# Kernel optimization log

Measured on AMD Instinct MI355X. Metric: run time of the kernel, lower is better.

The kernel has to match this reference:

```python
import jax, jax.numpy as jnp
import numpy as np

B, S, DM, H, DK, R, THETA = 8, 2048, 512, 8, 64, 128, 10000.0
BLK = R          # key/query block size; window radius == block size
NB = S // BLK    # number of blocks
NEG = -1e30      # additive mask for invalid positions (fp32-safe)


def setup_inputs() -> dict:
    key = jax.random.key(0)
    ks = jax.random.split(key, 5)
    scale = 0.02
    hidden_states = jax.random.normal(ks[0], (B, S, DM), jnp.float32)
    Wq = jax.random.normal(ks[1], (DM, H * DK), jnp.float32) * scale
    Wk = jax.random.normal(ks[2], (DM, H * DK), jnp.float32) * scale
    Wv = jax.random.normal(ks[3], (DM, H * DK), jnp.float32) * scale
    Wo = jax.random.normal(ks[4], (H * DK, DM), jnp.float32) * scale
    position_ids = jnp.tile(jnp.arange(S, dtype=jnp.int64)[None, :], (B, 1))
    return {"hidden_states": hidden_states, "Wq": Wq, "Wk": Wk, "Wv": Wv,
            "Wo": Wo, "position_ids": position_ids}


def _apply_rope(q, k, position_ids):
    # q,k: [B,H,S,DK]; position_ids: [B,S]
    half = DK // 2
    inv_freq = 1.0 / (THETA ** (jnp.arange(0, DK, 2, dtype=jnp.float32) / DK))  # [half]
    freqs = position_ids.astype(jnp.float32)[:, :, None] * inv_freq[None, None, :]  # [B,S,half]
    emb = jnp.concatenate([freqs, freqs], axis=-1)        # [B,S,DK]
    cos = jnp.cos(emb)[:, None, :, :]                     # [B,1,S,DK]
    sin = jnp.sin(emb)[:, None, :, :]

    def rotate_half(x):
        return jnp.concatenate([-x[..., half:], x[..., :half]], axis=-1)

    return q * cos + rotate_half(q) * sin, k * cos + rotate_half(k) * sin


def _band_mask():
    # valid[nb, BLK, 3*BLK]: key within [0,S) and |j - i| <= R
    b = jnp.arange(NB)[:, None, None]
    qi = jnp.arange(BLK)[None, :, None]
    kj = jnp.arange(3 * BLK)[None, None, :]
    kglob = (b - 1) * BLK + kj                 # global key index
    qglob = b * BLK + qi                        # global query index
    return (jnp.abs(kglob - qglob) <= R) & (kglob >= 0) & (kglob < S)


def reference(hidden_states, Wq, Wk, Wv, Wo, position_ids):
    # projections: [B,S,DM] -> [B,H,S,DK]
    def shape(x):
        return x.reshape(B, S, H, DK).transpose(0, 2, 1, 3)

    q = shape(hidden_states @ Wq)
    k = shape(hidden_states @ Wk)
    v = shape(hidden_states @ Wv)
    q, k = _apply_rope(q, k, position_ids)

    # block-banded sliding-window attention, softmax_scale = 1.0 (no scaling)
    pad = ((0, 0), (0, 0), (BLK, BLK), (0, 0))
    kb = jnp.pad(k, pad).reshape(B, H, NB + 2, BLK, DK)
    vb = jnp.pad(v, pad).reshape(B, H, NB + 2, BLK, DK)
    # neighbor window: blocks [b-1, b, b+1] -> [B,H,NB,3*BLK,DK]
    kwin = jnp.concatenate([kb[:, :, i:i + NB] for i in range(3)], axis=3)
    vwin = jnp.concatenate([vb[:, :, i:i + NB] for i in range(3)], axis=3)
    qb = q.reshape(B, H, NB, BLK, DK)

    scores = jnp.einsum('bhnqd,bhnkd->bhnqk', qb, kwin)   # unscaled
    valid = _band_mask()                                  # [NB,BLK,3*BLK]
    scores = jnp.where(valid[None, None], scores, NEG)
    attn = jax.nn.softmax(scores.astype(jnp.float32), axis=-1).astype(scores.dtype)
    outb = jnp.einsum('bhnqk,bhnkd->bhnqd', attn, vwin)   # [B,H,NB,BLK,DK]

    out = outb.reshape(B, H, S, DK).transpose(0, 2, 1, 3).reshape(B, S, H * DK)
    return out @ Wo
```

## Files before the change

kernel.cpp:

```cpp
#include <hip/hip_runtime.h>

using bf16 = __bf16;
typedef __bf16 bf16x8 __attribute__((ext_vector_type(8)));
typedef __bf16 bf16x4 __attribute__((ext_vector_type(4)));
typedef float f32x4 __attribute__((ext_vector_type(4)));
typedef float f32x16 __attribute__((ext_vector_type(16)));

#define MFMA16(a, b, c) __builtin_amdgcn_mfma_f32_16x16x32_bf16((a), (b), (c), 0, 0, 0)
#define MFMA32(a, b, c) __builtin_amdgcn_mfma_f32_32x32x16_bf16((a), (b), (c), 0, 0, 0)

constexpr int S = 2048, DM = 512, H = 8, DK = 64, HD = 512;
constexpr int NBLK = 16, BLK = 128;
constexpr int Mrows = 8 * S;
constexpr float LOG2E = 1.44269504088896340736f;

__device__ __forceinline__ void gll16(const void* g, void* l) {
  __builtin_amdgcn_global_load_lds((const __attribute__((address_space(1))) unsigned int*)g,
                                   (__attribute__((address_space(3))) unsigned int*)l, 16, 0, 0);
}

__global__ void k_conv(const float* __restrict__ x, bf16* __restrict__ y) {
  size_t i = ((size_t)blockIdx.x * 256 + threadIdx.x) * 8;
  float4 a = *(const float4*)(x + i);
  float4 b = *(const float4*)(x + i + 4);
  bf16x8 o;
  o[0] = (bf16)a.x; o[1] = (bf16)a.y; o[2] = (bf16)a.z; o[3] = (bf16)a.w;
  o[4] = (bf16)b.x; o[5] = (bf16)b.y; o[6] = (bf16)b.z; o[7] = (bf16)b.w;
  *(bf16x8*)(y + i) = o;
}

__global__ void k_transw4(const float* __restrict__ W0, const float* __restrict__ W1,
                          const float* __restrict__ W2, const float* __restrict__ W3,
                          bf16* __restrict__ D0, bf16* __restrict__ D1,
                          bf16* __restrict__ D2, bf16* __restrict__ D3) {
  const int z = blockIdx.z;
  const float* W = (z == 0) ? W0 : (z == 1) ? W1 : (z == 2) ? W2 : W3;
  bf16* Wt = (z == 0) ? D0 : (z == 1) ? D1 : (z == 2) ? D2 : D3;
  __shared__ float tile[32][33];
  int k0 = blockIdx.x * 32, n0 = blockIdx.y * 32;
  int tx = threadIdx.x, ty = threadIdx.y;
#pragma unroll
  for (int i = 0; i < 4; i++)
    tile[ty * 4 + i][tx] = W[(size_t)(k0 + ty * 4 + i) * 512 + n0 + tx];
  __syncthreads();
#pragma unroll
  for (int i = 0; i < 4; i++)
    Wt[(size_t)(n0 + ty * 4 + i) * 512 + k0 + tx] = (bf16)tile[tx][ty * 4 + i];
}

__global__ void k_ctab(float2* __restrict__ ctab) {
  int idx = blockIdx.x * 256 + threadIdx.x;
  int s = idx >> 5, i = idx & 31;
  float invf = exp2f(-(float)i * (13.287712379549449f / 32.0f));
  float ang = (float)s * invf;
  ctab[idx] = make_float2(cosf(ang), sinf(ang));
}

__global__ __launch_bounds__(256) void k_gemm_qkv(
    const bf16* __restrict__ Xb,
    const bf16* __restrict__ Wtq, const bf16* __restrict__ Wtk, const bf16* __restrict__ Wtv,
    bf16* __restrict__ Qo, bf16* __restrict__ Ko, bf16* __restrict__ Vt,
    const float2* __restrict__ ctab) {
  const int z = blockIdx.z;
  const bf16* Wt = (z == 0) ? Wtq : ((z == 1) ? Wtk : Wtv);
  bf16* dst = (z == 0) ? Qo : Ko;
  const float qscale = (z == 0) ? LOG2E : 1.0f;

  __shared__ __align__(16) char Asm[128 * 64];
  __shared__ __align__(16) char Bsm[128 * 64];

  const int t = threadIdx.x, l = t & 63, wid = t >> 6;
  const int l15 = l & 15, l4 = l >> 4;
  const int wm = wid >> 1, wn = wid & 1;
  const size_t arow0 = (size_t)blockIdx.x * 128;
  const size_t brow0 = (size_t)blockIdx.y * 128;

  f32x4 acc[4][4] = {};
  const int rs = wid * 16 + (l >> 2);
  const int cs = (l & 3) ^ ((l >> 2) & 3);

  for (int kt = 0; kt < 16; ++kt) {
    const int k0 = kt * 32;
    __syncthreads();
    gll16(Xb + (arow0 + rs) * 512 + k0 + cs * 8,      Asm + wid * 1024);
    gll16(Xb + (arow0 + 64 + rs) * 512 + k0 + cs * 8, Asm + 4096 + wid * 1024);
    gll16(Wt + (brow0 + rs) * 512 + k0 + cs * 8,      Bsm + wid * 1024);
    gll16(Wt + (brow0 + 64 + rs) * 512 + k0 + cs * 8, Bsm + 4096 + wid * 1024);
    __syncthreads();
    bf16x8 af[4], bfr[4];
#pragma unroll
    for (int mi = 0; mi < 4; mi++) {
      int row = wm * 64 + mi * 16 + l15;
      af[mi] = *(const bf16x8*)(Asm + row * 64 + ((l4 ^ (row & 3)) * 16));
    }
#pragma unroll
    for (int ni = 0; ni < 4; ni++) {
      int row = wn * 64 + ni * 16 + l15;
      bfr[ni] = *(const bf16x8*)(Bsm + row * 64 + ((l4 ^ (row & 3)) * 16));
    }
#pragma unroll
    for (int mi = 0; mi < 4; mi++)
#pragma unroll
      for (int ni = 0; ni < 4; ni++)
        acc[mi][ni] = MFMA16(af[mi], bfr[ni], acc[mi][ni]);
  }

  if (z == 2) {
    const int b = (int)(arow0 >> 11);
#pragma unroll
    for (int mi = 0; mi < 4; mi++) {
      int scol = (int)(arow0 & 2047) + wm * 64 + mi * 16 + l4 * 4;
#pragma unroll
      for (int ni = 0; ni < 4; ni++) {
        int col = (int)brow0 + wn * 64 + ni * 16 + l15;
        int hh = col >> 6, dd = col & 63;
        bf16x4 pk = {(bf16)acc[mi][ni][0], (bf16)acc[mi][ni][1],
                     (bf16)acc[mi][ni][2], (bf16)acc[mi][ni][3]};
        *(bf16x4*)(Vt + ((size_t)((b * H + hh) * 64 + dd)) * 2048 + scol) = pk;
      }
    }
    return;
  }

#pragma unroll
  for (int mi = 0; mi < 4; mi++) {
#pragma unroll
    for (int r = 0; r < 4; r++) {
      int grow = (int)arow0 + wm * 64 + mi * 16 + l4 * 4 + r;
      size_t rowoff = (size_t)grow * 512 + brow0 + wn * 64;
      int s = grow & (S - 1);
      float2 cs0 = ctab[s * 32 + l15];
      float2 cs1 = ctab[s * 32 + 16 + l15];
#pragma unroll
      for (int ni = 0; ni < 4; ni++) {
        float a = acc[mi][ni][r];
        float b = acc[mi][ni ^ 2][r];
        float2 cc = (ni & 1) ? cs1 : cs0;
        float val = (ni < 2) ? (a * cc.x - b * cc.y) : (a * cc.x + b * cc.y);
        dst[rowoff + ni * 16 + l15] = (bf16)(val * qscale);
      }
    }
  }
}

__global__ __launch_bounds__(256) void k_gemm_out(
    const bf16* __restrict__ A, const bf16* __restrict__ Wt, float* __restrict__ out) {
  __shared__ __align__(16) char Asm[128 * 64];
  __shared__ __align__(16) char Bsm[128 * 64];

  const int t = threadIdx.x, l = t & 63, wid = t >> 6;
  const int l15 = l & 15, l4 = l >> 4;
  const int wm = wid >> 1, wn = wid & 1;
  const size_t arow0 = (size_t)blockIdx.x * 128;
  const size_t brow0 = (size_t)blockIdx.y * 128;

  f32x4 acc[4][4] = {};
  const int rs = wid * 16 + (l >> 2);
  const int cs = (l & 3) ^ ((l >> 2) & 3);

  for (int kt = 0; kt < 16; ++kt) {
    const int k0 = kt * 32;
    __syncthreads();
    gll16(A + (arow0 + rs) * 512 + k0 + cs * 8,       Asm + wid * 1024);
    gll16(A + (arow0 + 64 + rs) * 512 + k0 + cs * 8,  Asm + 4096 + wid * 1024);
    gll16(Wt + (brow0 + rs) * 512 + k0 + cs * 8,      Bsm + wid * 1024);
    gll16(Wt + (brow0 + 64 + rs) * 512 + k0 + cs * 8, Bsm + 4096 + wid * 1024);
    __syncthreads();
    bf16x8 af[4], bfr[4];
#pragma unroll
    for (int mi = 0; mi < 4; mi++) {
      int row = wm * 64 + mi * 16 + l15;
      af[mi] = *(const bf16x8*)(Asm + row * 64 + ((l4 ^ (row & 3)) * 16));
    }
#pragma unroll
    for (int ni = 0; ni < 4; ni++) {
      int row = wn * 64 + ni * 16 + l15;
      bfr[ni] = *(const bf16x8*)(Bsm + row * 64 + ((l4 ^ (row & 3)) * 16));
    }
#pragma unroll
    for (int mi = 0; mi < 4; mi++)
#pragma unroll
      for (int ni = 0; ni < 4; ni++)
        acc[mi][ni] = MFMA16(af[mi], bfr[ni], acc[mi][ni]);
  }

#pragma unroll
  for (int mi = 0; mi < 4; mi++)
#pragma unroll
    for (int r = 0; r < 4; r++) {
      int grow = (int)arow0 + wm * 64 + mi * 16 + l4 * 4 + r;
      size_t rowoff = (size_t)grow * 512 + brow0 + wn * 64;
#pragma unroll
      for (int ni = 0; ni < 4; ni++)
        out[rowoff + ni * 16 + l15] = acc[mi][ni][r];
    }
}

__global__ __launch_bounds__(256, 4) void k_attn(
    const bf16* __restrict__ Q, const bf16* __restrict__ K, const bf16* __restrict__ Vt,
    bf16* __restrict__ O) {
  const int bid = blockIdx.x;
  const int swz = (bid & 7) * 128 + (bid >> 3);
  const int nb = swz & 15, h = (swz >> 4) & 7, bb = swz >> 7;
  const int t = threadIdx.x, l = t & 63, w = t >> 6;
  const int q31 = l & 31, hi = l >> 5;

  const int bh = bb * H + h;
  const size_t qrow = (size_t)bb * S + nb * BLK + w * 32 + q31;

  const bf16* Qp = Q + qrow * HD + h * DK + hi * 8;
  bf16x8 qb[4];
#pragma unroll
  for (int ks = 0; ks < 4; ks++) qb[ks] = *(const bf16x8*)(Qp + ks * 16);

  f32x16 o0 = {}, o1 = {};
  float mrun = -3e38f, lrun = 0.f;

  const bf16* Kbase = K + (size_t)bb * S * HD + h * DK + hi * 8;
  const bf16* Vbase = Vt + ((size_t)bh * 64 + q31) * 2048 + hi * 8;
  const int s0 = nb * BLK + w * 32 - 128;

  auto pv = [&](const f32x16& p, int kgc) {
    unsigned int Wd[4][2];
#pragma unroll
    for (int a = 0; a < 4; a++)
#pragma unroll
      for (int b2 = 0; b2 < 2; b2++) {
        unsigned int wd;
        asm("v_cvt_pk_bf16_f32 %0, %1, %2" : "=v"(wd) : "v"(p[4 * a + 2 * b2]), "v"(p[4 * a + 2 * b2 + 1]));
        Wd[a][b2] = wd;
      }
    bf16x8 pf[2];
#pragma unroll
    for (int ks = 0; ks < 2; ks++) {
      union { unsigned int u[4]; bf16x8 v; } cvt;
#pragma unroll
      for (int b2 = 0; b2 < 2; b2++) {
        unsigned int low_w = Wd[2 * ks][b2];
        unsigned int hi_w  = Wd[2 * ks + 1][b2];
        unsigned int msg = hi ? low_w : hi_w;
        unsigned int rec = __shfl_xor(msg, 32);
        cvt.u[b2]     = hi ? rec : low_w;
        cvt.u[2 + b2] = hi ? hi_w : rec;
      }
      pf[ks] = cvt.v;
    }
    const bf16* Vp = Vbase + kgc;
    o0 = MFMA32(*(const bf16x8*)(Vp), pf[0], o0);
    o0 = MFMA32(*(const bf16x8*)(Vp + 16), pf[1], o0);
    o1 = MFMA32(*(const bf16x8*)(Vp + 32 * 2048), pf[0], o1);
    o1 = MFMA32(*(const bf16x8*)(Vp + 32 * 2048 + 16), pf[1], o1);
  };

#pragma unroll
  for (int st = 0; st < 5; ++st) {
    const bool has2 = (st < 4);
    const int c0 = st * 2, c1 = c0 + 1;
    const int kg0 = s0 + c0 * 32, kg1 = s0 + c1 * 32;
    const int kc0 = kg0 < 0 ? 0 : (kg0 > S - 32 ? S - 32 : kg0);
    const int kc1 = kg1 < 0 ? 0 : (kg1 > S - 32 ? S - 32 : kg1);

    f32x16 a0 = {}, a1 = {};
    {
      const bf16* Kp = Kbase + (size_t)(kc0 + q31) * HD;
      a0 = MFMA32(*(const bf16x8*)(Kp),      qb[0], a0);
      a0 = MFMA32(*(const bf16x8*)(Kp + 16), qb[1], a0);
      a0 = MFMA32(*(const bf16x8*)(Kp + 32), qb[2], a0);
      a0 = MFMA32(*(const bf16x8*)(Kp + 48), qb[3], a0);
    }
    if (has2) {
      const bf16* Kp = Kbase + (size_t)(kc1 + q31) * HD;
      a1 = MFMA32(*(const bf16x8*)(Kp),      qb[0], a1);
      a1 = MFMA32(*(const bf16x8*)(Kp + 16), qb[1], a1);
      a1 = MFMA32(*(const bf16x8*)(Kp + 32), qb[2], a1);
      a1 = MFMA32(*(const bf16x8*)(Kp + 48), qb[3], a1);
    }

    if (kg0 != kc0) {
#pragma unroll
      for (int rg = 0; rg < 16; rg++) a0[rg] = -1e30f;
    } else if (c0 == 0) {
#pragma unroll
      for (int rg = 0; rg < 16; rg++) {
        int kk = (rg & 3) + 8 * (rg >> 2) + 4 * hi;
        if (kk < q31) a0[rg] = -1e30f;
      }
    } else if (c0 == 8) {
#pragma unroll
      for (int rg = 0; rg < 16; rg++) {
        int kk = (rg & 3) + 8 * (rg >> 2) + 4 * hi;
        if (kk > q31) a0[rg] = -1e30f;
      }
    }
    if (has2 && kg1 != kc1) {
#pragma unroll
      for (int rg = 0; rg < 16; rg++) a1[rg] = -1e30f;
    }

    f32x16 mx = a0;
    if (has2) {
#pragma unroll
      for (int rg = 0; rg < 16; rg++) mx[rg] = fmaxf(mx[rg], a1[rg]);
    }
#pragma unroll
    for (int sl = 8; sl >= 1; sl >>= 1)
#pragma unroll
      for (int i = 0; i < sl; i++) mx[i] = fmaxf(mx[i], mx[i + sl]);
    const float pm = fmaxf(mx[0], __shfl_xor(mx[0], 32));

    if (!__all(pm - mrun <= 8.0f)) {
      const float mnew = fmaxf(mrun, pm);
      const float alpha = exp2f(mrun - mnew);
      lrun *= alpha;
#pragma unroll
      for (int rg = 0; rg < 16; rg++) { o0[rg] *= alpha; o1[rg] *= alpha; }
      mrun = mnew;
    }

    float rsum = 0.f;
#pragma unroll
    for (int rg = 0; rg < 16; rg++) { a0[rg] = exp2f(a0[rg] - mrun); rsum += a0[rg]; }
    if (has2) {
#pragma unroll
      for (int rg = 0; rg < 16; rg++) { a1[rg] = exp2f(a1[rg] - mrun); rsum += a1[rg]; }
    }
    rsum += __shfl_xor(rsum, 32);
    lrun += rsum;

    pv(a0, kc0);
    if (has2) pv(a1, kc1);
  }

  const float inv = 1.0f / lrun;
  bf16* Op = O + qrow * HD + h * DK + 4 * hi;
#pragma unroll
  for (int dt = 0; dt < 2; dt++) {
    const f32x16 oo = dt ? o1 : o0;
#pragma unroll
    for (int a = 0; a < 4; a++) {
      bf16x4 ob = {(bf16)(oo[4 * a + 0] * inv), (bf16)(oo[4 * a + 1] * inv),
                   (bf16)(oo[4 * a + 2] * inv), (bf16)(oo[4 * a + 3] * inv)};
      *(bf16x4*)(Op + dt * 32 + 8 * a) = ob;
    }
  }
}

extern "C" void kernel_launch(void* const* d_in, const int* in_sizes, int n_in,
                              void* d_out, int out_size, void* d_ws, size_t ws_size,
                              hipStream_t stream) {
  const float* hs = (const float*)d_in[0];
  const float* Wq = (const float*)d_in[1];
  const float* Wk = (const float*)d_in[2];
  const float* Wv = (const float*)d_in[3];
  const float* Wo = (const float*)d_in[4];
  float* out = (float*)d_out;

  char* ws = (char*)d_ws;
  const size_t MB = 1u << 20;
  bf16* Xb = (bf16*)(ws);
  bf16* Qb = (bf16*)(ws + 16 * MB);
  bf16* Kb = (bf16*)(ws + 32 * MB);
  bf16* Vt = (bf16*)(ws + 48 * MB);
  bf16* Wtq = (bf16*)(ws + 64 * MB);
  bf16* Wtk = Wtq + 512 * 512;
  bf16* Wtv = Wtk + 512 * 512;
  bf16* Wto = Wtv + 512 * 512;
  float2* ctab = (float2*)(ws + 64 * MB + 4 * 512 * 512 * sizeof(bf16));
  bf16* AO = Xb;

  k_conv<<<dim3(Mrows * DM / (256 * 8)), dim3(256), 0, stream>>>(hs, Xb);
  k_transw4<<<dim3(16, 16, 4), dim3(32, 8), 0, stream>>>(Wq, Wk, Wv, Wo, Wtq, Wtk, Wtv, Wto);
  k_ctab<<<dim3(S * 32 / 256), dim3(256), 0, stream>>>(ctab);
  k_gemm_qkv<<<dim3(Mrows / 128, 4, 3), dim3(256), 0, stream>>>(Xb, Wtq, Wtk, Wtv, Qb, Kb, Vt, ctab);
  k_attn<<<dim3(NBLK * H * 8), dim3(256), 0, stream>>>(Qb, Kb, Vt, AO);
  k_gemm_out<<<dim3(Mrows / 128, 4), dim3(256), 0, stream>>>(AO, Wto, out);
}
```

Baseline: 117.2 us.

## Double-buffer GEMM LDS tiles and split attention keys across wave pairs

Both projection GEMMs now use double-buffered LDS. The next K-slice is issued through global_load_lds while MFMAs run on the current slice, so one barrier per iteration replaces two. The attention kernel now gives each 32-query group two waves: one handles the first two key chunk pairs and the other handles the rest. The partial softmax states are merged through LDS, which doubles the grid and raises occupancy (launch bounds 6). In exchange it adds LDS traffic and a block-wide sync for the merge, the load is uneven (2 vs 3 steps), and the LDS footprint per block grows.

```diff
diff --git a/kernel.cpp b/kernel.cpp
--- a/kernel.cpp
+++ b/kernel.cpp
@@ -66,8 +66,8 @@
   bf16* dst = (z == 0) ? Qo : Ko;
   const float qscale = (z == 0) ? LOG2E : 1.0f;
 
-  __shared__ __align__(16) char Asm[128 * 64];
-  __shared__ __align__(16) char Bsm[128 * 64];
+  __shared__ __align__(16) char Asm2[2][8192];
+  __shared__ __align__(16) char Bsm2[2][8192];
 
   const int t = threadIdx.x, l = t & 63, wid = t >> 6;
   const int l15 = l & 15, l4 = l >> 4;
@@ -79,30 +79,42 @@
   const int rs = wid * 16 + (l >> 2);
   const int cs = (l & 3) ^ ((l >> 2) & 3);
 
+  auto stage = [&](int kt, int b) {
+    const int k0 = kt * 32;
+    gll16(Xb + (arow0 + rs) * 512 + k0 + cs * 8,      Asm2[b] + wid * 1024);
+    gll16(Xb + (arow0 + 64 + rs) * 512 + k0 + cs * 8, Asm2[b] + 4096 + wid * 1024);
+    gll16(Wt + (brow0 + rs) * 512 + k0 + cs * 8,      Bsm2[b] + wid * 1024);
+    gll16(Wt + (brow0 + 64 + rs) * 512 + k0 + cs * 8, Bsm2[b] + 4096 + wid * 1024);
+  };
+
+  stage(0, 0);
+  asm volatile("s_waitcnt vmcnt(0)" ::: "memory");
+  __builtin_amdgcn_s_barrier();
+
+  int cur = 0;
   for (int kt = 0; kt < 16; ++kt) {
-    const int k0 = kt * 32;
-    __syncthreads();
-    gll16(Xb + (arow0 + rs) * 512 + k0 + cs * 8,      Asm + wid * 1024);
-    gll16(Xb + (arow0 + 64 + rs) * 512 + k0 + cs * 8, Asm + 4096 + wid * 1024);
-    gll16(Wt + (brow0 + rs) * 512 + k0 + cs * 8,      Bsm + wid * 1024);
-    gll16(Wt + (brow0 + 64 + rs) * 512 + k0 + cs * 8, Bsm + 4096 + wid * 1024);
-    __syncthreads();
+    if (kt < 15) stage(kt + 1, cur ^ 1);
     bf16x8 af[4], bfr[4];
 #pragma unroll
     for (int mi = 0; mi < 4; mi++) {
       int row = wm * 64 + mi * 16 + l15;
-      af[mi] = *(const bf16x8*)(Asm + row * 64 + ((l4 ^ (row & 3)) * 16));
+      af[mi] = *(const bf16x8*)(Asm2[cur] + row * 64 + ((l4 ^ (row & 3)) * 16));
     }
 #pragma unroll
     for (int ni = 0; ni < 4; ni++) {
       int row = wn * 64 + ni * 16 + l15;
-      bfr[ni] = *(const bf16x8*)(Bsm + row * 64 + ((l4 ^ (row & 3)) * 16));
+      bfr[ni] = *(const bf16x8*)(Bsm2[cur] + row * 64 + ((l4 ^ (row & 3)) * 16));
     }
 #pragma unroll
     for (int mi = 0; mi < 4; mi++)
 #pragma unroll
       for (int ni = 0; ni < 4; ni++)
         acc[mi][ni] = MFMA16(af[mi], bfr[ni], acc[mi][ni]);
+    if (kt < 15) {
+      asm volatile("s_waitcnt vmcnt(0)" ::: "memory");
+      __builtin_amdgcn_s_barrier();
+    }
+    cur ^= 1;
   }
 
   if (z == 2) {
@@ -145,8 +157,8 @@
 
 __global__ __launch_bounds__(256) void k_gemm_out(
     const bf16* __restrict__ A, const bf16* __restrict__ Wt, float* __restrict__ out) {
-  __shared__ __align__(16) char Asm[128 * 64];
-  __shared__ __align__(16) char Bsm[128 * 64];
+  __shared__ __align__(16) char Asm2[2][8192];
+  __shared__ __align__(16) char Bsm2[2][8192];
 
   const int t = threadIdx.x, l = t & 63, wid = t >> 6;
   const int l15 = l & 15, l4 = l >> 4;
@@ -158,30 +170,42 @@
   const int rs = wid * 16 + (l >> 2);
   const int cs = (l & 3) ^ ((l >> 2) & 3);
 
+  auto stage = [&](int kt, int b) {
+    const int k0 = kt * 32;
+    gll16(A + (arow0 + rs) * 512 + k0 + cs * 8,       Asm2[b] + wid * 1024);
+    gll16(A + (arow0 + 64 + rs) * 512 + k0 + cs * 8,  Asm2[b] + 4096 + wid * 1024);
+    gll16(Wt + (brow0 + rs) * 512 + k0 + cs * 8,      Bsm2[b] + wid * 1024);
+    gll16(Wt + (brow0 + 64 + rs) * 512 + k0 + cs * 8, Bsm2[b] + 4096 + wid * 1024);
+  };
+
+  stage(0, 0);
+  asm volatile("s_waitcnt vmcnt(0)" ::: "memory");
+  __builtin_amdgcn_s_barrier();
+
+  int cur = 0;
   for (int kt = 0; kt < 16; ++kt) {
-    const int k0 = kt * 32;
-    __syncthreads();
-    gll16(A + (arow0 + rs) * 512 + k0 + cs * 8,       Asm + wid * 1024);
-    gll16(A + (arow0 + 64 + rs) * 512 + k0 + cs * 8,  Asm + 4096 + wid * 1024);
-    gll16(Wt + (brow0 + rs) * 512 + k0 + cs * 8,      Bsm + wid * 1024);
-    gll16(Wt + (brow0 + 64 + rs) * 512 + k0 + cs * 8, Bsm + 4096 + wid * 1024);
-    __syncthreads();
+    if (kt < 15) stage(kt + 1, cur ^ 1);
     bf16x8 af[4], bfr[4];
 #pragma unroll
     for (int mi = 0; mi < 4; mi++) {
       int row = wm * 64 + mi * 16 + l15;
-      af[mi] = *(const bf16x8*)(Asm + row * 64 + ((l4 ^ (row & 3)) * 16));
+      af[mi] = *(const bf16x8*)(Asm2[cur] + row * 64 + ((l4 ^ (row & 3)) * 16));
     }
 #pragma unroll
     for (int ni = 0; ni < 4; ni++) {
       int row = wn * 64 + ni * 16 + l15;
-      bfr[ni] = *(const bf16x8*)(Bsm + row * 64 + ((l4 ^ (row & 3)) * 16));
+      bfr[ni] = *(const bf16x8*)(Bsm2[cur] + row * 64 + ((l4 ^ (row & 3)) * 16));
     }
 #pragma unroll
     for (int mi = 0; mi < 4; mi++)
 #pragma unroll
       for (int ni = 0; ni < 4; ni++)
         acc[mi][ni] = MFMA16(af[mi], bfr[ni], acc[mi][ni]);
+    if (kt < 15) {
+      asm volatile("s_waitcnt vmcnt(0)" ::: "memory");
+      __builtin_amdgcn_s_barrier();
+    }
+    cur ^= 1;
   }
 
 #pragma unroll
@@ -196,29 +220,34 @@
     }
 }
 
-__global__ __launch_bounds__(256, 4) void k_attn(
+__global__ __launch_bounds__(256, 6) void k_attn(
     const bf16* __restrict__ Q, const bf16* __restrict__ K, const bf16* __restrict__ Vt,
     bf16* __restrict__ O) {
   const int bid = blockIdx.x;
-  const int swz = (bid & 7) * 128 + (bid >> 3);
-  const int nb = swz & 15, h = (swz >> 4) & 7, bb = swz >> 7;
+  const int swz = (bid & 7) * 256 + (bid >> 3);
+  const int qg = swz & 31, h = (swz >> 5) & 7, bb = swz >> 8;
   const int t = threadIdx.x, l = t & 63, w = t >> 6;
+  const int sub = w & 1, half = w >> 1;
   const int q31 = l & 31, hi = l >> 5;
 
+  __shared__ float Osm[2][64][34];
+  __shared__ float Mlm[2][64][2];
+
   const int bh = bb * H + h;
-  const size_t qrow = (size_t)bb * S + nb * BLK + w * 32 + q31;
+  const int qbase = qg * 64 + sub * 32;
+  const size_t qrow = (size_t)bb * S + qbase + q31;
 
   const bf16* Qp = Q + qrow * HD + h * DK + hi * 8;
-  bf16x8 qb[4];
-#pragma unroll
-  for (int ks = 0; ks < 4; ks++) qb[ks] = *(const bf16x8*)(Qp + ks * 16);
+  bf16x8 qb4[4];
+#pragma unroll
+  for (int ks = 0; ks < 4; ks++) qb4[ks] = *(const bf16x8*)(Qp + ks * 16);
 
   f32x16 o0 = {}, o1 = {};
   float mrun = -3e38f, lrun = 0.f;
 
   const bf16* Kbase = K + (size_t)bb * S * HD + h * DK + hi * 8;
   const bf16* Vbase = Vt + ((size_t)bh * 64 + q31) * 2048 + hi * 8;
-  const int s0 = nb * BLK + w * 32 - 128;
+  const int s0 = qbase - 128;
 
   auto pv = [&](const f32x16& p, int kgc) {
     unsigned int Wd[4][2];
@@ -252,40 +281,38 @@
     o1 = MFMA32(*(const bf16x8*)(Vp + 32 * 2048 + 16), pf[1], o1);
   };
 
-#pragma unroll
-  for (int st = 0; st < 5; ++st) {
-    const bool has2 = (st < 4);
-    const int c0 = st * 2, c1 = c0 + 1;
-    const int kg0 = s0 + c0 * 32, kg1 = s0 + c1 * 32;
+  auto step2 = [&](int c0, bool has2, bool triL, bool triR) {
+    const int kg0 = s0 + c0 * 32, kg1 = kg0 + 32;
+    if ((has2 ? kg1 : kg0) < 0 || kg0 > S - 32) return;
     const int kc0 = kg0 < 0 ? 0 : (kg0 > S - 32 ? S - 32 : kg0);
     const int kc1 = kg1 < 0 ? 0 : (kg1 > S - 32 ? S - 32 : kg1);
 
     f32x16 a0 = {}, a1 = {};
     {
       const bf16* Kp = Kbase + (size_t)(kc0 + q31) * HD;
-      a0 = MFMA32(*(const bf16x8*)(Kp),      qb[0], a0);
-      a0 = MFMA32(*(const bf16x8*)(Kp + 16), qb[1], a0);
-      a0 = MFMA32(*(const bf16x8*)(Kp + 32), qb[2], a0);
-      a0 = MFMA32(*(const bf16x8*)(Kp + 48), qb[3], a0);
+      a0 = MFMA32(*(const bf16x8*)(Kp),      qb4[0], a0);
+      a0 = MFMA32(*(const bf16x8*)(Kp + 16), qb4[1], a0);
+      a0 = MFMA32(*(const bf16x8*)(Kp + 32), qb4[2], a0);
+      a0 = MFMA32(*(const bf16x8*)(Kp + 48), qb4[3], a0);
     }
     if (has2) {
       const bf16* Kp = Kbase + (size_t)(kc1 + q31) * HD;
-      a1 = MFMA32(*(const bf16x8*)(Kp),      qb[0], a1);
-      a1 = MFMA32(*(const bf16x8*)(Kp + 16), qb[1], a1);
-      a1 = MFMA32(*(const bf16x8*)(Kp + 32), qb[2], a1);
-      a1 = MFMA32(*(const bf16x8*)(Kp + 48), qb[3], a1);
+      a1 = MFMA32(*(const bf16x8*)(Kp),      qb4[0], a1);
+      a1 = MFMA32(*(const bf16x8*)(Kp + 16), qb4[1], a1);
+      a1 = MFMA32(*(const bf16x8*)(Kp + 32), qb4[2], a1);
+      a1 = MFMA32(*(const bf16x8*)(Kp + 48), qb4[3], a1);
     }
 
     if (kg0 != kc0) {
 #pragma unroll
       for (int rg = 0; rg < 16; rg++) a0[rg] = -1e30f;
-    } else if (c0 == 0) {
+    } else if (triL) {
 #pragma unroll
       for (int rg = 0; rg < 16; rg++) {
         int kk = (rg & 3) + 8 * (rg >> 2) + 4 * hi;
         if (kk < q31) a0[rg] = -1e30f;
       }
-    } else if (c0 == 8) {
+    } else if (triR) {
 #pragma unroll
       for (int rg = 0; rg < 16; rg++) {
         int kk = (rg & 3) + 8 * (rg >> 2) + 4 * hi;
@@ -329,18 +356,51 @@
 
     pv(a0, kc0);
     if (has2) pv(a1, kc1);
-  }
-
-  const float inv = 1.0f / lrun;
-  bf16* Op = O + qrow * HD + h * DK + 4 * hi;
-#pragma unroll
-  for (int dt = 0; dt < 2; dt++) {
-    const f32x16 oo = dt ? o1 : o0;
-#pragma unroll
-    for (int a = 0; a < 4; a++) {
-      bf16x4 ob = {(bf16)(oo[4 * a + 0] * inv), (bf16)(oo[4 * a + 1] * inv),
-                   (bf16)(oo[4 * a + 2] * inv), (bf16)(oo[4 * a + 3] * inv)};
-      *(bf16x4*)(Op + dt * 32 + 8 * a) = ob;
+  };
+
+  if (half == 0) {
+    step2(0, true, true, false);
+    step2(2, true, false, false);
+  } else {
+    step2(4, true, false, false);
+    step2(6, true, false, false);
+    step2(8, false, false, true);
+  }
+
+  if (half == 1) {
+#pragma unroll
+    for (int dt = 0; dt < 2; dt++) {
+      const f32x16 oo = dt ? o1 : o0;
+#pragma unroll
+      for (int j = 0; j < 8; j++)
+        *(float2*)&Osm[sub][l][dt * 16 + 2 * j] = make_float2(oo[2 * j], oo[2 * j + 1]);
+    }
+    Mlm[sub][l][0] = mrun;
+    Mlm[sub][l][1] = lrun;
+  }
+  __syncthreads();
+  if (half == 0) {
+    const float m1 = Mlm[sub][l][0], l1 = Mlm[sub][l][1];
+    const float mstar = fmaxf(mrun, m1);
+    const float sa = exp2f(mrun - mstar), sb = exp2f(m1 - mstar);
+    const float inv = 1.0f / (lrun * sa + l1 * sb);
+    const float c0 = sa * inv, c1 = sb * inv;
+    bf16* Op = O + qrow * HD + h * DK + 4 * hi;
+#pragma unroll
+    for (int dt = 0; dt < 2; dt++) {
+      const f32x16 oo = dt ? o1 : o0;
+      float mg[16];
+#pragma unroll
+      for (int j = 0; j < 8; j++) {
+        float2 pp = *(float2*)&Osm[sub][l][dt * 16 + 2 * j];
+        mg[2 * j]     = oo[2 * j] * c0 + pp.x * c1;
+        mg[2 * j + 1] = oo[2 * j + 1] * c0 + pp.y * c1;
+      }
+#pragma unroll
+      for (int a = 0; a < 4; a++) {
+        bf16x4 ob = {(bf16)mg[4 * a], (bf16)mg[4 * a + 1], (bf16)mg[4 * a + 2], (bf16)mg[4 * a + 3]};
+        *(bf16x4*)(Op + dt * 32 + 8 * a) = ob;
+      }
     }
   }
 }
@@ -372,6 +432,6 @@
   k_transw4<<<dim3(16, 16, 4), dim3(32, 8), 0, stream>>>(Wq, Wk, Wv, Wo, Wtq, Wtk, Wtv, Wto);
   k_ctab<<<dim3(S * 32 / 256), dim3(256), 0, stream>>>(ctab);
   k_gemm_qkv<<<dim3(Mrows / 128, 4, 3), dim3(256), 0, stream>>>(Xb, Wtq, Wtk, Wtv, Qb, Kb, Vt, ctab);
-  k_attn<<<dim3(NBLK * H * 8), dim3(256), 0, stream>>>(Qb, Kb, Vt, AO);
+  k_attn<<<dim3(2048), dim3(256), 0, stream>>>(Qb, Kb, Vt, AO);
   k_gemm_out<<<dim3(Mrows / 128, 4), dim3(256), 0, stream>>>(AO, Wto, out);
 }
```

After: 169.0 us. 44.2% more time.

## Double-buffer LDS in projection GEMMs and remap blocks for XCD locality

Applied to the files above, without the earlier changes.

Both GEMM kernels now use two LDS buffers, so the global->LDS load of the next K tile is issued before the MFMAs on the current tile, with one wait and barrier per iteration instead of two syncthreads. The grids are flattened to 1D and blocks are remapped so each XCD (bid&7) handles a contiguous range of 16 row tiles across all N tiles and Q/K/V, aiming to improve L2 reuse of the shared A rows. LDS use doubles to 32KB per block, which may reduce occupancy.

```diff
diff --git a/kernel.cpp b/kernel.cpp
--- a/kernel.cpp
+++ b/kernel.cpp
@@ -61,48 +61,63 @@
     const bf16* __restrict__ Wtq, const bf16* __restrict__ Wtk, const bf16* __restrict__ Wtv,
     bf16* __restrict__ Qo, bf16* __restrict__ Ko, bf16* __restrict__ Vt,
     const float2* __restrict__ ctab) {
-  const int z = blockIdx.z;
+  const int bid = blockIdx.x;
+  const int xcd = bid & 7, i = bid >> 3;
+  const int mloc = i / 12, zy = i % 12;
+  const int z = zy >> 2, y = zy & 3;
   const bf16* Wt = (z == 0) ? Wtq : ((z == 1) ? Wtk : Wtv);
   bf16* dst = (z == 0) ? Qo : Ko;
   const float qscale = (z == 0) ? LOG2E : 1.0f;
 
-  __shared__ __align__(16) char Asm[128 * 64];
-  __shared__ __align__(16) char Bsm[128 * 64];
+  __shared__ __align__(16) char Asm2[2][8192];
+  __shared__ __align__(16) char Bsm2[2][8192];
 
   const int t = threadIdx.x, l = t & 63, wid = t >> 6;
   const int l15 = l & 15, l4 = l >> 4;
   const int wm = wid >> 1, wn = wid & 1;
-  const size_t arow0 = (size_t)blockIdx.x * 128;
-  const size_t brow0 = (size_t)blockIdx.y * 128;
+  const size_t arow0 = (size_t)(xcd * 16 + mloc) * 128;
+  const size_t brow0 = (size_t)y * 128;
 
   f32x4 acc[4][4] = {};
   const int rs = wid * 16 + (l >> 2);
   const int cs = (l & 3) ^ ((l >> 2) & 3);
 
+  auto stage = [&](int kt, int b) {
+    const int k0 = kt * 32;
+    gll16(Xb + (arow0 + rs) * 512 + k0 + cs * 8,      Asm2[b] + wid * 1024);
+    gll16(Xb + (arow0 + 64 + rs) * 512 + k0 + cs * 8, Asm2[b] + 4096 + wid * 1024);
+    gll16(Wt + (brow0 + rs) * 512 + k0 + cs * 8,      Bsm2[b] + wid * 1024);
+    gll16(Wt + (brow0 + 64 + rs) * 512 + k0 + cs * 8, Bsm2[b] + 4096 + wid * 1024);
+  };
+
+  stage(0, 0);
+  asm volatile("s_waitcnt vmcnt(0)" ::: "memory");
+  __builtin_amdgcn_s_barrier();
+
+  int cur = 0;
   for (int kt = 0; kt < 16; ++kt) {
-    const int k0 = kt * 32;
-    __syncthreads();
-    gll16(Xb + (arow0 + rs) * 512 + k0 + cs * 8,      Asm + wid * 1024);
-    gll16(Xb + (arow0 + 64 + rs) * 512 + k0 + cs * 8, Asm + 4096 + wid * 1024);
-    gll16(Wt + (brow0 + rs) * 512 + k0 + cs * 8,      Bsm + wid * 1024);
-    gll16(Wt + (brow0 + 64 + rs) * 512 + k0 + cs * 8, Bsm + 4096 + wid * 1024);
-    __syncthreads();
+    if (kt < 15) stage(kt + 1, cur ^ 1);
     bf16x8 af[4], bfr[4];
 #pragma unroll
     for (int mi = 0; mi < 4; mi++) {
       int row = wm * 64 + mi * 16 + l15;
-      af[mi] = *(const bf16x8*)(Asm + row * 64 + ((l4 ^ (row & 3)) * 16));
+      af[mi] = *(const bf16x8*)(Asm2[cur] + row * 64 + ((l4 ^ (row & 3)) * 16));
     }
 #pragma unroll
     for (int ni = 0; ni < 4; ni++) {
       int row = wn * 64 + ni * 16 + l15;
-      bfr[ni] = *(const bf16x8*)(Bsm + row * 64 + ((l4 ^ (row & 3)) * 16));
+      bfr[ni] = *(const bf16x8*)(Bsm2[cur] + row * 64 + ((l4 ^ (row & 3)) * 16));
     }
 #pragma unroll
     for (int mi = 0; mi < 4; mi++)
 #pragma unroll
       for (int ni = 0; ni < 4; ni++)
         acc[mi][ni] = MFMA16(af[mi], bfr[ni], acc[mi][ni]);
+    if (kt < 15) {
+      asm volatile("s_waitcnt vmcnt(0)" ::: "memory");
+      __builtin_amdgcn_s_barrier();
+    }
+    cur ^= 1;
   }
 
   if (z == 2) {
@@ -145,43 +160,57 @@
 
 __global__ __launch_bounds__(256) void k_gemm_out(
     const bf16* __restrict__ A, const bf16* __restrict__ Wt, float* __restrict__ out) {
-  __shared__ __align__(16) char Asm[128 * 64];
-  __shared__ __align__(16) char Bsm[128 * 64];
+  const int bid = blockIdx.x;
+  const int xcd = bid & 7, i = bid >> 3;
+  __shared__ __align__(16) char Asm2[2][8192];
+  __shared__ __align__(16) char Bsm2[2][8192];
 
   const int t = threadIdx.x, l = t & 63, wid = t >> 6;
   const int l15 = l & 15, l4 = l >> 4;
   const int wm = wid >> 1, wn = wid & 1;
-  const size_t arow0 = (size_t)blockIdx.x * 128;
-  const size_t brow0 = (size_t)blockIdx.y * 128;
+  const size_t arow0 = (size_t)(xcd * 16 + (i >> 2)) * 128;
+  const size_t brow0 = (size_t)(i & 3) * 128;
 
   f32x4 acc[4][4] = {};
   const int rs = wid * 16 + (l >> 2);
   const int cs = (l & 3) ^ ((l >> 2) & 3);
 
+  auto stage = [&](int kt, int b) {
+    const int k0 = kt * 32;
+    gll16(A + (arow0 + rs) * 512 + k0 + cs * 8,       Asm2[b] + wid * 1024);
+    gll16(A + (arow0 + 64 + rs) * 512 + k0 + cs * 8,  Asm2[b] + 4096 + wid * 1024);
+    gll16(Wt + (brow0 + rs) * 512 + k0 + cs * 8,      Bsm2[b] + wid * 1024);
+    gll16(Wt + (brow0 + 64 + rs) * 512 + k0 + cs * 8, Bsm2[b] + 4096 + wid * 1024);
+  };
+
+  stage(0, 0);
+  asm volatile("s_waitcnt vmcnt(0)" ::: "memory");
+  __builtin_amdgcn_s_barrier();
+
+  int cur = 0;
   for (int kt = 0; kt < 16; ++kt) {
-    const int k0 = kt * 32;
-    __syncthreads();
-    gll16(A + (arow0 + rs) * 512 + k0 + cs * 8,       Asm + wid * 1024);
-    gll16(A + (arow0 + 64 + rs) * 512 + k0 + cs * 8,  Asm + 4096 + wid * 1024);
-    gll16(Wt + (brow0 + rs) * 512 + k0 + cs * 8,      Bsm + wid * 1024);
-    gll16(Wt + (brow0 + 64 + rs) * 512 + k0 + cs * 8, Bsm + 4096 + wid * 1024);
-    __syncthreads();
+    if (kt < 15) stage(kt + 1, cur ^ 1);
     bf16x8 af[4], bfr[4];
 #pragma unroll
     for (int mi = 0; mi < 4; mi++) {
       int row = wm * 64 + mi * 16 + l15;
-      af[mi] = *(const bf16x8*)(Asm + row * 64 + ((l4 ^ (row & 3)) * 16));
+      af[mi] = *(const bf16x8*)(Asm2[cur] + row * 64 + ((l4 ^ (row & 3)) * 16));
     }
 #pragma unroll
     for (int ni = 0; ni < 4; ni++) {
       int row = wn * 64 + ni * 16 + l15;
-      bfr[ni] = *(const bf16x8*)(Bsm + row * 64 + ((l4 ^ (row & 3)) * 16));
+      bfr[ni] = *(const bf16x8*)(Bsm2[cur] + row * 64 + ((l4 ^ (row & 3)) * 16));
     }
 #pragma unroll
     for (int mi = 0; mi < 4; mi++)
 #pragma unroll
       for (int ni = 0; ni < 4; ni++)
         acc[mi][ni] = MFMA16(af[mi], bfr[ni], acc[mi][ni]);
+    if (kt < 15) {
+      asm volatile("s_waitcnt vmcnt(0)" ::: "memory");
+      __builtin_amdgcn_s_barrier();
+    }
+    cur ^= 1;
   }
 
 #pragma unroll
@@ -305,7 +334,7 @@
 #pragma unroll
     for (int sl = 8; sl >= 1; sl >>= 1)
 #pragma unroll
-      for (int i = 0; i < sl; i++) mx[i] = fmaxf(mx[i], mx[i + sl]);
+      for (int i2 = 0; i2 < sl; i2++) mx[i2] = fmaxf(mx[i2], mx[i2 + sl]);
     const float pm = fmaxf(mx[0], __shfl_xor(mx[0], 32));
 
     if (!__all(pm - mrun <= 8.0f)) {
@@ -371,7 +400,7 @@
   k_conv<<<dim3(Mrows * DM / (256 * 8)), dim3(256), 0, stream>>>(hs, Xb);
   k_transw4<<<dim3(16, 16, 4), dim3(32, 8), 0, stream>>>(Wq, Wk, Wv, Wo, Wtq, Wtk, Wtv, Wto);
   k_ctab<<<dim3(S * 32 / 256), dim3(256), 0, stream>>>(ctab);
-  k_gemm_qkv<<<dim3(Mrows / 128, 4, 3), dim3(256), 0, stream>>>(Xb, Wtq, Wtk, Wtv, Qb, Kb, Vt, ctab);
+  k_gemm_qkv<<<dim3(1536), dim3(256), 0, stream>>>(Xb, Wtq, Wtk, Wtv, Qb, Kb, Vt, ctab);
   k_attn<<<dim3(NBLK * H * 8), dim3(256), 0, stream>>>(Qb, Kb, Vt, AO);
-  k_gemm_out<<<dim3(Mrows / 128, 4), dim3(256), 0, stream>>>(AO, Wto, out);
-}
+  k_gemm_out<<<dim3(512), dim3(256), 0, stream>>>(AO, Wto, out);
+}
```

Result: slower. 124.7 us (+6.4%).
